# Kernel tuning notes

Hardware: AMD Instinct MI355X
Metric: run time of the kernel (lower is better)

The kernel has to match this reference:

```python
import jax, jax.numpy as jnp
import numpy as np

MAX_LEN = 3

def _attention(h, enc, w1, b1, w2):
    # h: [B,H], enc: [B,S,H]
    B, S, H = enc.shape
    hs = jnp.broadcast_to(h[:, None, :], (B, S, H))
    x = jnp.tanh(jnp.concatenate([enc, hs], axis=-1) @ w1.T + b1)  # [B,S,H]
    e = (x @ w2.T)[..., 0]                                         # [B,S]
    alpha = jax.nn.softmax(e, axis=1)
    return jnp.einsum('bs,bsd->bd', alpha, enc)                    # [B,H]

def _gru_cell(x, h, w_ih, w_hh, b_ih, b_hh):
    # torch GRU gate order: r, z, n
    H = h.shape[-1]
    gi = x @ w_ih.T + b_ih   # [B,3H]
    gh = h @ w_hh.T + b_hh
    i_r, i_z, i_n = gi[:, :H], gi[:, H:2*H], gi[:, 2*H:]
    h_r, h_z, h_n = gh[:, :H], gh[:, H:2*H], gh[:, 2*H:]
    r = jax.nn.sigmoid(i_r + h_r)
    z = jax.nn.sigmoid(i_z + h_z)
    n = jnp.tanh(i_n + r * h_n)
    return (1.0 - z) * n + z * h

def setup_inputs() -> dict:
    key = jax.random.key(0)
    ks = jax.random.split(key, 16)
    B, S, H, DW = 1024, 40, 1024, 512
    V0 = V1 = 4000
    EMB_N = V0 + V1 + 1
    sc = lambda fan: 1.0 / np.sqrt(fan)
    inp = {
        'encoder_outputs': jax.random.normal(ks[0], (B, S, H), jnp.float32),
        'encoder_hidden': jax.random.normal(ks[1], (1, B, H), jnp.float32),
        'targets': jax.random.randint(ks[2], (MAX_LEN, B), 0, V0),
        'emb': jax.random.normal(ks[3], (EMB_N, DW), jnp.float32) * 0.02,
        'attn_w1': jax.random.normal(ks[4], (H, 2 * H), jnp.float32) * sc(2 * H),
        'attn_b1': jnp.zeros((H,), jnp.float32),
        'attn_w2': jax.random.normal(ks[5], (1, H), jnp.float32) * sc(H),
        'w_ih': jax.random.normal(ks[6], (3 * H, H + DW), jnp.float32) * sc(H),
        'w_hh': jax.random.normal(ks[7], (3 * H, H), jnp.float32) * sc(H),
        'b_ih': jnp.zeros((3 * H,), jnp.float32),
        'b_hh': jnp.zeros((3 * H,), jnp.float32),
        'out0_w': jax.random.normal(ks[8], (V0, H), jnp.float32) * sc(H),
        'out0_b': jnp.zeros((V0,), jnp.float32),
        'out1_w': jax.random.normal(ks[9], (V1, H), jnp.float32) * sc(H),
        'out1_b': jnp.zeros((V1,), jnp.float32),
    }
    return inp

def reference(encoder_outputs, encoder_hidden, targets, emb, attn_w1, attn_b1,
              attn_w2, w_ih, w_hh, b_ih, b_hh, out0_w, out0_b, out1_w, out1_b):
    B = encoder_outputs.shape[0]
    h = encoder_hidden[0]  # n_layers=1, unidirectional -> init state passthrough
    logs = []
    for t in range(MAX_LEN):
        context = _attention(h, encoder_outputs, attn_w1, attn_b1, attn_w2)
        if t == 0:
            it = jnp.zeros((B,), jnp.int32)
        elif t == 1:
            it = targets[0] + 1
        else:
            it = targets[t - 1] + 36
        x = jnp.concatenate([emb[it], context], axis=1)  # [B, DW+H]
        h = _gru_cell(x, h, w_ih, w_hh, b_ih, b_hh)
        if t == 0 or t == 2:
            logits = h @ out0_w.T + out0_b
        else:
            logits = h @ out1_w.T + out1_b
        logs.append(jax.nn.log_softmax(logits, axis=1))
    return jnp.stack(logs)  # [MAX_LEN, B, V]
```

## Files before the change

### kernel.cpp

```cpp
#include <hip/hip_runtime.h>
#include <hip/hip_bf16.h>
#include <math.h>

#define B_SZ 1024
#define S_SZ 40
#define H_SZ 1024
#define DW_SZ 512
#define V_SZ 4000
#define XW (DW_SZ + H_SZ)
#define NG (4 * H_SZ)

typedef __bf16 bf16x8 __attribute__((ext_vector_type(8)));
typedef float f32x4 __attribute__((ext_vector_type(4)));

__device__ __forceinline__ float fast_tanh(float x) {
    return 1.0f - 2.0f / (1.0f + __expf(2.0f * x));
}
__device__ __forceinline__ float fast_sigmoid(float x) {
    return 1.0f / (1.0f + __expf(-x));
}
__device__ __forceinline__ float bfraw2f(unsigned short u) {
    return __uint_as_float(((unsigned)u) << 16);
}

#define GLL16(gp, lp)                                                                \
    __builtin_amdgcn_global_load_lds((const __attribute__((address_space(1))) void*)(gp), \
                                     (__attribute__((address_space(3))) void*)(lp), 16, 0, 0)

__global__ __launch_bounds__(256, 2) void gemm_bt_pipe128(
    const __hip_bfloat16* __restrict__ A, int lda,
    const __hip_bfloat16* __restrict__ W, int ldw,
    __hip_bfloat16* __restrict__ C, int ldc,
    int nbx, int K) {
    extern __shared__ char smem[];
    const int tid = threadIdx.x;
    const int lane = tid & 63;
    const int wave = tid >> 6;
    const int wm = wave >> 1, wn = wave & 1;
    const int fr = lane & 15, fq = lane >> 4;

    int bid = blockIdx.x;
    { const int cpx = gridDim.x >> 3; bid = (bid & 7) * cpx + (bid >> 3); }
    const int by = bid / nbx;
    const int bm = by * 128;
    const int bn = (bid - by * nbx) * 256;

    const int r0 = tid >> 2;
    const int s0 = (tid & 3) ^ ((tid >> 3) & 3);
    const __hip_bfloat16* gA0 = A + (size_t)(bm + r0) * lda + s0 * 8;
    const __hip_bfloat16* gA1 = A + (size_t)(bm + r0 + 64) * lda + s0 * 8;
    const __hip_bfloat16* gW0 = W + (size_t)(bn + r0) * ldw + s0 * 8;
    const __hip_bfloat16* gW1 = W + (size_t)(bn + r0 + 64) * ldw + s0 * 8;
    const __hip_bfloat16* gW2 = W + (size_t)(bn + r0 + 128) * ldw + s0 * 8;
    const __hip_bfloat16* gW3 = W + (size_t)(bn + r0 + 192) * ldw + s0 * 8;
    const int dst0 = tid * 16;

    int aoff[4], boff[8];
#pragma unroll
    for (int mi = 0; mi < 4; ++mi) {
        const int row = wm * 64 + mi * 16 + fr;
        aoff[mi] = row * 64 + ((fq ^ ((row >> 1) & 3)) << 4);
    }
#pragma unroll
    for (int ni = 0; ni < 8; ++ni) {
        const int col = wn * 128 + ni * 16 + fr;
        boff[ni] = 8192 + col * 64 + ((fq ^ ((col >> 1) & 3)) << 4);
    }

    const int NT = K >> 5;
    f32x4 acc[4][8] = {};

#define STAGE_T(t)                                                    \
    do {                                                              \
        char* sb = smem + ((t) % 3) * 24576;                          \
        const int kk = (t) << 5;                                      \
        GLL16(gA0 + kk, sb + dst0);                                   \
        GLL16(gA1 + kk, sb + dst0 + 4096);                            \
        GLL16(gW0 + kk, sb + 8192 + dst0);                            \
        GLL16(gW1 + kk, sb + 8192 + dst0 + 4096);                     \
        GLL16(gW2 + kk, sb + 8192 + dst0 + 8192);                     \
        GLL16(gW3 + kk, sb + 8192 + dst0 + 12288);                    \
    } while (0)

    STAGE_T(0);
    STAGE_T(1);
    __builtin_amdgcn_sched_barrier(0);
    asm volatile("s_waitcnt vmcnt(6)" ::: "memory");
    __builtin_amdgcn_s_barrier();
    __builtin_amdgcn_sched_barrier(0);

    for (int t = 0; t < NT; ++t) {
        if (t + 2 < NT) STAGE_T(t + 2);

        const char* sb = smem + (t % 3) * 24576;
        bf16x8 af[4], bg[8];
#pragma unroll
        for (int ni = 0; ni < 8; ++ni) bg[ni] = *reinterpret_cast<const bf16x8*>(sb + boff[ni]);
#pragma unroll
        for (int mi = 0; mi < 4; ++mi) af[mi] = *reinterpret_cast<const bf16x8*>(sb + aoff[mi]);

        __builtin_amdgcn_s_setprio(1);
#pragma unroll
        for (int mi = 0; mi < 4; ++mi)
#pragma unroll
            for (int ni = 0; ni < 8; ++ni)
                acc[mi][ni] = __builtin_amdgcn_mfma_f32_16x16x32_bf16(af[mi], bg[ni], acc[mi][ni], 0, 0, 0);
        __builtin_amdgcn_s_setprio(0);

        if (t != NT - 1) {
            __builtin_amdgcn_sched_barrier(0);
            if (t + 2 < NT) asm volatile("s_waitcnt vmcnt(6)" ::: "memory");
            else            asm volatile("s_waitcnt vmcnt(0)" ::: "memory");
            __builtin_amdgcn_s_barrier();
            __builtin_amdgcn_sched_barrier(0);
        }
    }
#undef STAGE_T

#pragma unroll
    for (int mi = 0; mi < 4; ++mi) {
        const int row0 = bm + wm * 64 + mi * 16 + fq * 4;
#pragma unroll
        for (int ni = 0; ni < 8; ++ni) {
            const int col = bn + wn * 128 + ni * 16 + fr;
#pragma unroll
            for (int r = 0; r < 4; ++r)
                C[(size_t)(row0 + r) * ldc + col] = __float2bfloat16(acc[mi][ni][r]);
        }
    }
}

template <int OB, int SWZ>
__global__ __launch_bounds__(256) void gemm_bt_mfma(
    const __hip_bfloat16* __restrict__ A, int lda,
    const __hip_bfloat16* __restrict__ W, int ldw,
    const float* __restrict__ bias,
    void* __restrict__ Cv, int ldc,
    int nbx, int N, int K) {
    __shared__ __align__(16) __hip_bfloat16 As[128 * 32];
    __shared__ __align__(16) __hip_bfloat16 Ws[128 * 32];
    const int tid = threadIdx.x;
    const int lane = tid & 63;
    const int wave = tid >> 6;

    int bid = blockIdx.x;
    if (SWZ) {
        const int cpx = gridDim.x >> 3;
        bid = (bid & 7) * cpx + (bid >> 3);
    }
    const int by = bid / nbx;
    const int bx = bid - by * nbx;
    const int bm = by * 128;
    const int bn = bx * 128;

    const int r0 = tid >> 2;
    const int kk = (tid & 3) * 8;
    const __hip_bfloat16* gA0 = A + (size_t)(bm + r0) * lda + kk;
    const __hip_bfloat16* gA1 = gA0 + (size_t)64 * lda;
    int wrow0 = bn + r0;      if (wrow0 > N - 1) wrow0 = N - 1;
    int wrow1 = bn + r0 + 64; if (wrow1 > N - 1) wrow1 = N - 1;
    const __hip_bfloat16* gW0 = W + (size_t)wrow0 * ldw + kk;
    const __hip_bfloat16* gW1 = W + (size_t)wrow1 * ldw + kk;
    char* As_c = (char*)As + tid * 16;
    char* Ws_c = (char*)Ws + tid * 16;

    const int wr = wave >> 1, wc = wave & 1;
    const int fr = lane & 15, fq = lane >> 4;
    const __hip_bfloat16* Ard = &As[(wr * 64 + fr) * 32 + fq * 8];
    const __hip_bfloat16* Wrd = &Ws[(wc * 64 + fr) * 32 + fq * 8];

    f32x4 acc[4][4] = {};

    for (int k0 = 0; k0 < K; k0 += 32) {
        __syncthreads();
        GLL16(gA0 + k0, As_c);
        GLL16(gA1 + k0, As_c + 4096);
        GLL16(gW0 + k0, Ws_c);
        GLL16(gW1 + k0, Ws_c + 4096);
        __syncthreads();

        bf16x8 af[4], bg[4];
#pragma unroll
        for (int i = 0; i < 4; ++i) {
            af[i] = *reinterpret_cast<const bf16x8*>(Ard + i * 16 * 32);
            bg[i] = *reinterpret_cast<const bf16x8*>(Wrd + i * 16 * 32);
        }
#pragma unroll
        for (int mi = 0; mi < 4; ++mi)
#pragma unroll
            for (int ni = 0; ni < 4; ++ni)
                acc[mi][ni] = __builtin_amdgcn_mfma_f32_16x16x32_bf16(af[mi], bg[ni], acc[mi][ni], 0, 0, 0);
    }

#pragma unroll
    for (int ni = 0; ni < 4; ++ni) {
        const int col = bn + wc * 64 + ni * 16 + fr;
        if (col >= N) continue;
        const float bb = bias ? bias[col] : 0.0f;
#pragma unroll
        for (int mi = 0; mi < 4; ++mi) {
            const int row0 = bm + wr * 64 + mi * 16 + fq * 4;
#pragma unroll
            for (int r = 0; r < 4; ++r) {
                const float v = acc[mi][ni][r] + bb;
                if (OB)
                    reinterpret_cast<__hip_bfloat16*>(Cv)[(size_t)(row0 + r) * ldc + col] = __float2bfloat16(v);
                else
                    reinterpret_cast<float*>(Cv)[(size_t)(row0 + r) * ldc + col] = v;
            }
        }
    }
}

__global__ __launch_bounds__(256) void gemm_dual_mfma(
    const __hip_bfloat16* __restrict__ A,
    const __hip_bfloat16* __restrict__ Wg,
    const __hip_bfloat16* __restrict__ Wo,
    const float* __restrict__ bias_cat,
    const float* __restrict__ ob,
    __hip_bfloat16* __restrict__ hg,
    float* __restrict__ logits,
    int full) {
    const int nbx = 64;
    const int bid = blockIdx.x;
    const int by = bid / nbx;
    const int bx = bid - by * nbx;
    const int bm = by * 128;
    const int bn = bx * 128;
    const int is_hg = (bn < NG);
    if (!full && is_hg) return;

    __shared__ __align__(16) __hip_bfloat16 As[128 * 32];
    __shared__ __align__(16) __hip_bfloat16 Ws[128 * 32];
    const int tid = threadIdx.x;
    const int lane = tid & 63;
    const int wave = tid >> 6;

    const __hip_bfloat16* Wb = is_hg ? Wg : Wo;
    const int coff = is_hg ? bn : bn - NG;
    const int nn = is_hg ? NG : V_SZ;

    const int r0 = tid >> 2;
    const int kk = (tid & 3) * 8;
    const __hip_bfloat16* gA0 = A + (size_t)(bm + r0) * H_SZ + kk;
    const __hip_bfloat16* gA1 = gA0 + (size_t)64 * H_SZ;
    int wrow0 = coff + r0;      if (wrow0 > nn - 1) wrow0 = nn - 1;
    int wrow1 = coff + r0 + 64; if (wrow1 > nn - 1) wrow1 = nn - 1;
    const __hip_bfloat16* gW0 = Wb + (size_t)wrow0 * H_SZ + kk;
    const __hip_bfloat16* gW1 = Wb + (size_t)wrow1 * H_SZ + kk;
    char* As_c = (char*)As + tid * 16;
    char* Ws_c = (char*)Ws + tid * 16;

    const int wr = wave >> 1, wc = wave & 1;
    const int fr = lane & 15, fq = lane >> 4;
    const __hip_bfloat16* Ard = &As[(wr * 64 + fr) * 32 + fq * 8];
    const __hip_bfloat16* Wrd = &Ws[(wc * 64 + fr) * 32 + fq * 8];

    f32x4 acc[4][4] = {};

    for (int k0 = 0; k0 < H_SZ; k0 += 32) {
        __syncthreads();
        GLL16(gA0 + k0, As_c);
        GLL16(gA1 + k0, As_c + 4096);
        GLL16(gW0 + k0, Ws_c);
        GLL16(gW1 + k0, Ws_c + 4096);
        __syncthreads();

        bf16x8 af[4], bg[4];
#pragma unroll
        for (int i = 0; i < 4; ++i) {
            af[i] = *reinterpret_cast<const bf16x8*>(Ard + i * 16 * 32);
            bg[i] = *reinterpret_cast<const bf16x8*>(Wrd + i * 16 * 32);
        }
#pragma unroll
        for (int mi = 0; mi < 4; ++mi)
#pragma unroll
            for (int ni = 0; ni < 4; ++ni)
                acc[mi][ni] = __builtin_amdgcn_mfma_f32_16x16x32_bf16(af[mi], bg[ni], acc[mi][ni], 0, 0, 0);
    }

#pragma unroll
    for (int ni = 0; ni < 4; ++ni) {
        const int cl = coff + wc * 64 + ni * 16 + fr;
        if (cl >= nn) continue;
        const float bb = is_hg ? bias_cat[cl] : ob[cl];
#pragma unroll
        for (int mi = 0; mi < 4; ++mi) {
            const int row0 = bm + wr * 64 + mi * 16 + fq * 4;
#pragma unroll
            for (int r = 0; r < 4; ++r) {
                const float v = acc[mi][ni][r] + bb;
                if (is_hg)
                    hg[(size_t)(row0 + r) * NG + cl] = __float2bfloat16(v);
                else
                    logits[(size_t)(row0 + r) * V_SZ + cl] = v;
            }
        }
    }
}

__global__ __launch_bounds__(256) void cast_f32_to_bf16(
    const float* __restrict__ src, long long sstride, int cols,
    __hip_bfloat16* __restrict__ dst, int nrows) {
    const int c4n = cols >> 2;
    const long long total4 = (long long)nrows * c4n;
    for (long long i = (long long)blockIdx.x * 256 + threadIdx.x; i < total4;
         i += (long long)gridDim.x * 256) {
        const long long r = i / c4n;
        const int c = (int)(i - r * c4n) << 2;
        const float4 v = *reinterpret_cast<const float4*>(src + r * sstride + c);
        union { ushort4 u; __hip_bfloat16 h[4]; } o;
        o.h[0] = __float2bfloat16(v.x); o.h[1] = __float2bfloat16(v.y);
        o.h[2] = __float2bfloat16(v.z); o.h[3] = __float2bfloat16(v.w);
        *reinterpret_cast<ushort4*>(dst + r * (long long)cols + c) = o.u;
    }
}

struct CastSeg { const float* src; long long sstride; int c4n; __hip_bfloat16* dst; long long n4; };
__global__ __launch_bounds__(256) void cast_all_kernel(CastSeg s0, CastSeg s1, CastSeg s2,
                                                       CastSeg s3, CastSeg s4, CastSeg s5) {
    const long long e0 = s0.n4, e1 = e0 + s1.n4, e2 = e1 + s2.n4,
                    e3 = e2 + s3.n4, e4 = e3 + s4.n4, e5 = e4 + s5.n4;
    for (long long i = (long long)blockIdx.x * 256 + threadIdx.x; i < e5;
         i += (long long)gridDim.x * 256) {
        CastSeg sg; long long li = i;
        if (i < e0) { sg = s0; }
        else if (i < e1) { sg = s1; li -= e0; }
        else if (i < e2) { sg = s2; li -= e1; }
        else if (i < e3) { sg = s3; li -= e2; }
        else if (i < e4) { sg = s4; li -= e3; }
        else { sg = s5; li -= e4; }
        const long long r = li / sg.c4n;
        const int c = (int)(li - r * sg.c4n) << 2;
        const float4 v = *reinterpret_cast<const float4*>(sg.src + r * sg.sstride + c);
        union { ushort4 u; __hip_bfloat16 h[4]; } o;
        o.h[0] = __float2bfloat16(v.x); o.h[1] = __float2bfloat16(v.y);
        o.h[2] = __float2bfloat16(v.z); o.h[3] = __float2bfloat16(v.w);
        *reinterpret_cast<ushort4*>(sg.dst + r * (long long)(sg.c4n << 2) + c) = o.u;
    }
}

__global__ __launch_bounds__(256) void build_bias_cat(
    const float* __restrict__ b1, const float* __restrict__ b_hh,
    float* __restrict__ dst) {
    const int j = blockIdx.x * 256 + threadIdx.x;
    dst[j] = (j < H_SZ) ? b1[j] : b_hh[j - H_SZ];
}

__global__ __launch_bounds__(256) void h_init_kernel(
    const float* __restrict__ enc_h, float* __restrict__ h, __hip_bfloat16* __restrict__ h_bf) {
    const int i = blockIdx.x * 256 + threadIdx.x;
    const float4 v = reinterpret_cast<const float4*>(enc_h)[i];
    reinterpret_cast<float4*>(h)[i] = v;
    union { ushort4 u; __hip_bfloat16 hh[4]; } o;
    o.hh[0] = __float2bfloat16(v.x); o.hh[1] = __float2bfloat16(v.y);
    o.hh[2] = __float2bfloat16(v.z); o.hh[3] = __float2bfloat16(v.w);
    reinterpret_cast<ushort4*>(h_bf)[i] = o.u;
}

__global__ __launch_bounds__(128) void emb_prefill_kernel(
    const float* __restrict__ emb,
    const int* __restrict__ targets,
    __hip_bfloat16* __restrict__ x0,
    __hip_bfloat16* __restrict__ x1,
    __hip_bfloat16* __restrict__ x2) {
    const int blk = blockIdx.x;
    const int t = blk >> 10;
    const int b = blk & 1023;
    const int tid = threadIdx.x;
    int it;
    __hip_bfloat16* x;
    if (t == 0) { it = 0; x = x0; }
    else if (t == 1) { it = targets[b] + 1; x = x1; }
    else { it = targets[B_SZ + b] + 36; x = x2; }
    float4 v = reinterpret_cast<const float4*>(emb + (size_t)it * DW_SZ)[tid];
    union { ushort4 u; __hip_bfloat16 h[4]; } o;
    o.h[0] = __float2bfloat16(v.x); o.h[1] = __float2bfloat16(v.y);
    o.h[2] = __float2bfloat16(v.z); o.h[3] = __float2bfloat16(v.w);
    reinterpret_cast<ushort4*>(x + (size_t)b * XW)[tid] = o.u;
}

__global__ __launch_bounds__(256) void attn_ctx_kernel(
    const __hip_bfloat16* __restrict__ enc,
    const __hip_bfloat16* __restrict__ enc_proj,
    const __hip_bfloat16* __restrict__ hg,
    const float* __restrict__ w2,
    __hip_bfloat16* __restrict__ x) {
    const int b = blockIdx.x;
    const int tid = threadIdx.x;
    const int lane = tid & 63, wave = tid >> 6;
    __shared__ float s_e[S_SZ];

    float hp[16], wv[16];
    const unsigned short* hgrow = reinterpret_cast<const unsigned short*>(hg) + (size_t)b * NG;
#pragma unroll
    for (int p = 0; p < 4; ++p) {
        const int base = p * 256 + lane * 4;
        ushort4 hu = *reinterpret_cast<const ushort4*>(hgrow + base);
        float4 wq = *reinterpret_cast<const float4*>(w2 + base);
        hp[p * 4 + 0] = bfraw2f(hu.x); hp[p * 4 + 1] = bfraw2f(hu.y);
        hp[p * 4 + 2] = bfraw2f(hu.z); hp[p * 4 + 3] = bfraw2f(hu.w);
        wv[p * 4 + 0] = wq.x; wv[p * 4 + 1] = wq.y;
        wv[p * 4 + 2] = wq.z; wv[p * 4 + 3] = wq.w;
    }

    const unsigned short* ep0 = reinterpret_cast<const unsigned short*>(enc_proj) + (size_t)b * S_SZ * H_SZ;
#pragma unroll 2
    for (int i = 0; i < 10; ++i) {
        const int s = wave + 4 * i;
        const unsigned short* row = ep0 + (size_t)s * H_SZ;
        float acc = 0.f;
#pragma unroll
        for (int p = 0; p < 4; ++p) {
            ushort4 eu = *reinterpret_cast<const ushort4*>(row + p * 256 + lane * 4);
            acc += fast_tanh(bfraw2f(eu.x) + hp[p * 4 + 0]) * wv[p * 4 + 0]
                 + fast_tanh(bfraw2f(eu.y) + hp[p * 4 + 1]) * wv[p * 4 + 1]
                 + fast_tanh(bfraw2f(eu.z) + hp[p * 4 + 2]) * wv[p * 4 + 2]
                 + fast_tanh(bfraw2f(eu.w) + hp[p * 4 + 3]) * wv[p * 4 + 3];
        }
#pragma unroll
        for (int off = 32; off > 0; off >>= 1) acc += __shfl_down(acc, off);
        if (lane == 0) s_e[s] = acc;
    }
    __syncthreads();

    float m = -1e30f;
    for (int s = 0; s < S_SZ; ++s) m = fmaxf(m, s_e[s]);
    float sum = 0.f;
    for (int s = 0; s < S_SZ; ++s) sum += __expf(s_e[s] - m);
    const float inv = 1.0f / sum;

    const ushort4* enc_b = reinterpret_cast<const ushort4*>(enc + (size_t)b * S_SZ * H_SZ);
    float4 acc = make_float4(0.f, 0.f, 0.f, 0.f);
    for (int s = 0; s < S_SZ; ++s) {
        const float a = __expf(s_e[s] - m) * inv;
        ushort4 ev = enc_b[s * 256 + tid];
        acc.x += a * bfraw2f(ev.x); acc.y += a * bfraw2f(ev.y);
        acc.z += a * bfraw2f(ev.z); acc.w += a * bfraw2f(ev.w);
    }
    union { ushort4 u; __hip_bfloat16 h[4]; } o;
    o.h[0] = __float2bfloat16(acc.x); o.h[1] = __float2bfloat16(acc.y);
    o.h[2] = __float2bfloat16(acc.z); o.h[3] = __float2bfloat16(acc.w);
    reinterpret_cast<ushort4*>(x + (size_t)b * XW + DW_SZ)[tid] = o.u;
}

__global__ __launch_bounds__(256) void gru_gate_kernel(
    const __hip_bfloat16* __restrict__ gi,
    const __hip_bfloat16* __restrict__ hg,
    float* __restrict__ h,
    __hip_bfloat16* __restrict__ h_bf) {
    const int idx = blockIdx.x * 256 + threadIdx.x;
    const int b = idx >> 10;
    const int j = idx & 1023;
    const unsigned short* gib = reinterpret_cast<const unsigned short*>(gi) + (size_t)b * 3 * H_SZ;
    const unsigned short* ghb = reinterpret_cast<const unsigned short*>(hg) + (size_t)b * NG + H_SZ;
    const float i_r = bfraw2f(gib[j]), i_z = bfraw2f(gib[H_SZ + j]), i_n = bfraw2f(gib[2 * H_SZ + j]);
    const float h_r = bfraw2f(ghb[j]), h_z = bfraw2f(ghb[H_SZ + j]), h_n = bfraw2f(ghb[2 * H_SZ + j]);
    const float r = fast_sigmoid(i_r + h_r);
    const float z = fast_sigmoid(i_z + h_z);
    const float n = fast_tanh(i_n + r * h_n);
    const float hv = (1.0f - z) * n + z * h[idx];
    h[idx] = hv;
    h_bf[idx] = __float2bfloat16(hv);
}

__global__ __launch_bounds__(256) void logsoftmax_kernel(float* __restrict__ buf) {
    const int b = blockIdx.x;
    const int tid = threadIdx.x;
    const int lane = tid & 63, wave = tid >> 6;
    __shared__ float s_red[4];
    __shared__ float s_bc;
    float* row = buf + (size_t)b * V_SZ;

    float m = -1e30f;
    for (int k = tid; k < V_SZ; k += 256) m = fmaxf(m, row[k]);
#pragma unroll
    for (int off = 32; off > 0; off >>= 1) m = fmaxf(m, __shfl_down(m, off));
    if (lane == 0) s_red[wave] = m;
    __syncthreads();
    if (tid == 0) s_bc = fmaxf(fmaxf(s_red[0], s_red[1]), fmaxf(s_red[2], s_red[3]));
    __syncthreads();
    m = s_bc;

    float sum = 0.f;
    for (int k = tid; k < V_SZ; k += 256) sum += expf(row[k] - m);
#pragma unroll
    for (int off = 32; off > 0; off >>= 1) sum += __shfl_down(sum, off);
    __syncthreads();
    if (lane == 0) s_red[wave] = sum;
    __syncthreads();
    if (tid == 0) s_bc = logf(s_red[0] + s_red[1] + s_red[2] + s_red[3]) + m;
    __syncthreads();
    const float ls = s_bc;

    for (int k = tid; k < V_SZ; k += 256) row[k] = row[k] - ls;
}

extern "C" void kernel_launch(void* const* d_in, const int* in_sizes, int n_in,
                              void* d_out, int out_size, void* d_ws, size_t ws_size,
                              hipStream_t stream) {
    const float* enc    = (const float*)d_in[0];
    const float* enc_h  = (const float*)d_in[1];
    const int*   tgt    = (const int*)d_in[2];
    const float* emb    = (const float*)d_in[3];
    const float* w1     = (const float*)d_in[4];
    const float* b1     = (const float*)d_in[5];
    const float* w2     = (const float*)d_in[6];
    const float* w_ih   = (const float*)d_in[7];
    const float* w_hh   = (const float*)d_in[8];
    const float* b_ih   = (const float*)d_in[9];
    const float* b_hh   = (const float*)d_in[10];
    const float* out0_w = (const float*)d_in[11];
    const float* out0_b = (const float*)d_in[12];
    const float* out1_w = (const float*)d_in[13];
    const float* out1_b = (const float*)d_in[14];
    float* out = (float*)d_out;

    char* wp = (char*)d_ws;
    auto carve = [&](size_t bytes) { char* p = wp; wp += (bytes + 255) & ~(size_t)255; return p; };
    __hip_bfloat16* enc_bf  = (__hip_bfloat16*)carve((size_t)B_SZ * S_SZ * H_SZ * 2);
    __hip_bfloat16* encp_bf = (__hip_bfloat16*)carve((size_t)B_SZ * S_SZ * H_SZ * 2);
    __hip_bfloat16* w1a_bf  = (__hip_bfloat16*)carve((size_t)H_SZ * H_SZ * 2);
    __hip_bfloat16* wcat_bf = (__hip_bfloat16*)carve((size_t)NG * H_SZ * 2);
    __hip_bfloat16* wih_bf  = (__hip_bfloat16*)carve((size_t)3 * H_SZ * XW * 2);
    __hip_bfloat16* o0_bf   = (__hip_bfloat16*)carve((size_t)V_SZ * H_SZ * 2);
    __hip_bfloat16* o1_bf   = (__hip_bfloat16*)carve((size_t)V_SZ * H_SZ * 2);
    float*          bias_cat= (float*)carve((size_t)NG * 4);
    float*          h       = (float*)carve((size_t)B_SZ * H_SZ * 4);
    __hip_bfloat16* h_bf    = (__hip_bfloat16*)carve((size_t)B_SZ * H_SZ * 2);
    __hip_bfloat16* hg_bf   = (__hip_bfloat16*)carve((size_t)B_SZ * NG * 2);
    __hip_bfloat16* x_bf[3];
    for (int t = 0; t < 3; ++t) x_bf[t] = (__hip_bfloat16*)carve((size_t)B_SZ * XW * 2);
    __hip_bfloat16* gi_bf   = (__hip_bfloat16*)carve((size_t)B_SZ * 3 * H_SZ * 2);

    cast_f32_to_bf16<<<2048, 256, 0, stream>>>(enc, H_SZ, H_SZ, enc_bf, B_SZ * S_SZ);
    {
        CastSeg s0{w1,            2 * H_SZ, H_SZ / 4, w1a_bf,                        (long long)H_SZ * H_SZ / 4};
        CastSeg s1{w1 + H_SZ,     2 * H_SZ, H_SZ / 4, wcat_bf,                       (long long)H_SZ * H_SZ / 4};
        CastSeg s2{w_hh,          H_SZ,     H_SZ / 4, wcat_bf + (size_t)H_SZ * H_SZ, (long long)3 * H_SZ * H_SZ / 4};
        CastSeg s3{w_ih,          XW,       XW / 4,   wih_bf,                        (long long)3 * H_SZ * XW / 4};
        CastSeg s4{out0_w,        H_SZ,     H_SZ / 4, o0_bf,                         (long long)V_SZ * H_SZ / 4};
        CastSeg s5{out1_w,        H_SZ,     H_SZ / 4, o1_bf,                         (long long)V_SZ * H_SZ / 4};
        cast_all_kernel<<<2048, 256, 0, stream>>>(s0, s1, s2, s3, s4, s5);
    }
    build_bias_cat<<<NG / 256, 256, 0, stream>>>(b1, b_hh, bias_cat);
    emb_prefill_kernel<<<3 * B_SZ, 128, 0, stream>>>(emb, tgt, x_bf[0], x_bf[1], x_bf[2]);
    h_init_kernel<<<(B_SZ * H_SZ / 4) / 256, 256, 0, stream>>>(enc_h, h, h_bf);

    gemm_bt_pipe128<<<(B_SZ * S_SZ / 128) * (H_SZ / 256), 256, 3 * 24576, stream>>>(
        enc_bf, H_SZ, w1a_bf, H_SZ, encp_bf, H_SZ, H_SZ / 256, H_SZ);

    gemm_bt_mfma<1, 0><<<(B_SZ / 128) * (NG / 128), 256, 0, stream>>>(
        h_bf, H_SZ, wcat_bf, H_SZ, bias_cat, hg_bf, NG, NG / 128, NG, H_SZ);

    for (int t = 0; t < 3; ++t) {
        attn_ctx_kernel<<<B_SZ, 256, 0, stream>>>(enc_bf, encp_bf, hg_bf, w2, x_bf[t]);

        gemm_bt_mfma<1, 0><<<(B_SZ / 128) * (3 * H_SZ / 128), 256, 0, stream>>>(
            x_bf[t], XW, wih_bf, XW, b_ih, gi_bf, 3 * H_SZ, 3 * H_SZ / 128, 3 * H_SZ, XW);

        gru_gate_kernel<<<(B_SZ * H_SZ) / 256, 256, 0, stream>>>(gi_bf, hg_bf, h, h_bf);

        float* logits = out + (size_t)t * B_SZ * V_SZ;
        const __hip_bfloat16* ow = (t == 1) ? o1_bf : o0_bf;
        const float* ob = (t == 1) ? out1_b : out0_b;
        gemm_dual_mfma<<<(B_SZ / 128) * 64, 256, 0, stream>>>(
            h_bf, wcat_bf, ow, bias_cat, ob, hg_bf, logits, (t < 2) ? 1 : 0);

        logsoftmax_kernel<<<B_SZ, 256, 0, stream>>>(logits);
    }
}
```

Before: 556.7 us.

## Fuse attention with log-softmax, merge prep kernels, store logits as bf16

Fuses the next step's attention-context kernel and the current step's log-softmax into one launch with block-range dispatch. Logits are written as bf16 to a scratch buffer and expanded to fp32 during log-softmax, which cuts fp32 round-trip traffic. Folds the encoder cast into cast_all_kernel and merges the embedding prefill, h init and bias concat into one kernel, removing several launches. It also moves the GEMM prefetch stage after the LDS fragment reads, and it adds bf16 rounding error to the logits.

```diff
diff --git a/kernel.cpp b/kernel.cpp
--- a/kernel.cpp
+++ b/kernel.cpp
@@ -90,14 +90,14 @@
     __builtin_amdgcn_sched_barrier(0);
 
     for (int t = 0; t < NT; ++t) {
-        if (t + 2 < NT) STAGE_T(t + 2);
-
         const char* sb = smem + (t % 3) * 24576;
         bf16x8 af[4], bg[8];
 #pragma unroll
         for (int ni = 0; ni < 8; ++ni) bg[ni] = *reinterpret_cast<const bf16x8*>(sb + boff[ni]);
 #pragma unroll
         for (int mi = 0; mi < 4; ++mi) af[mi] = *reinterpret_cast<const bf16x8*>(sb + aoff[mi]);
+
+        if (t + 2 < NT) STAGE_T(t + 2);
 
         __builtin_amdgcn_s_setprio(1);
 #pragma unroll
@@ -219,7 +219,7 @@
     const float* __restrict__ bias_cat,
     const float* __restrict__ ob,
     __hip_bfloat16* __restrict__ hg,
-    float* __restrict__ logits,
+    __hip_bfloat16* __restrict__ lg,
     int full) {
     const int nbx = 64;
     const int bid = blockIdx.x;
@@ -293,35 +293,18 @@
                 if (is_hg)
                     hg[(size_t)(row0 + r) * NG + cl] = __float2bfloat16(v);
                 else
-                    logits[(size_t)(row0 + r) * V_SZ + cl] = v;
+                    lg[(size_t)(row0 + r) * V_SZ + cl] = __float2bfloat16(v);
             }
         }
-    }
-}
-
-__global__ __launch_bounds__(256) void cast_f32_to_bf16(
-    const float* __restrict__ src, long long sstride, int cols,
-    __hip_bfloat16* __restrict__ dst, int nrows) {
-    const int c4n = cols >> 2;
-    const long long total4 = (long long)nrows * c4n;
-    for (long long i = (long long)blockIdx.x * 256 + threadIdx.x; i < total4;
-         i += (long long)gridDim.x * 256) {
-        const long long r = i / c4n;
-        const int c = (int)(i - r * c4n) << 2;
-        const float4 v = *reinterpret_cast<const float4*>(src + r * sstride + c);
-        union { ushort4 u; __hip_bfloat16 h[4]; } o;
-        o.h[0] = __float2bfloat16(v.x); o.h[1] = __float2bfloat16(v.y);
-        o.h[2] = __float2bfloat16(v.z); o.h[3] = __float2bfloat16(v.w);
-        *reinterpret_cast<ushort4*>(dst + r * (long long)cols + c) = o.u;
     }
 }
 
 struct CastSeg { const float* src; long long sstride; int c4n; __hip_bfloat16* dst; long long n4; };
 __global__ __launch_bounds__(256) void cast_all_kernel(CastSeg s0, CastSeg s1, CastSeg s2,
-                                                       CastSeg s3, CastSeg s4, CastSeg s5) {
+                                                       CastSeg s3, CastSeg s4, CastSeg s5, CastSeg s6) {
     const long long e0 = s0.n4, e1 = e0 + s1.n4, e2 = e1 + s2.n4,
-                    e3 = e2 + s3.n4, e4 = e3 + s4.n4, e5 = e4 + s5.n4;
-    for (long long i = (long long)blockIdx.x * 256 + threadIdx.x; i < e5;
+                    e3 = e2 + s3.n4, e4 = e3 + s4.n4, e5 = e4 + s5.n4, e6 = e5 + s6.n4;
+    for (long long i = (long long)blockIdx.x * 256 + threadIdx.x; i < e6;
          i += (long long)gridDim.x * 256) {
         CastSeg sg; long long li = i;
         if (i < e0) { sg = s0; }
@@ -329,7 +312,8 @@
         else if (i < e2) { sg = s2; li -= e1; }
         else if (i < e3) { sg = s3; li -= e2; }
         else if (i < e4) { sg = s4; li -= e3; }
-        else { sg = s5; li -= e4; }
+        else if (i < e5) { sg = s5; li -= e4; }
+        else { sg = s6; li -= e5; }
         const long long r = li / sg.c4n;
         const int c = (int)(li - r * sg.c4n) << 2;
         const float4 v = *reinterpret_cast<const float4*>(sg.src + r * sg.sstride + c);
@@ -340,108 +324,150 @@
     }
 }
 
-__global__ __launch_bounds__(256) void build_bias_cat(
-    const float* __restrict__ b1, const float* __restrict__ b_hh,
-    float* __restrict__ dst) {
-    const int j = blockIdx.x * 256 + threadIdx.x;
-    dst[j] = (j < H_SZ) ? b1[j] : b_hh[j - H_SZ];
-}
-
-__global__ __launch_bounds__(256) void h_init_kernel(
-    const float* __restrict__ enc_h, float* __restrict__ h, __hip_bfloat16* __restrict__ h_bf) {
-    const int i = blockIdx.x * 256 + threadIdx.x;
-    const float4 v = reinterpret_cast<const float4*>(enc_h)[i];
-    reinterpret_cast<float4*>(h)[i] = v;
-    union { ushort4 u; __hip_bfloat16 hh[4]; } o;
-    o.hh[0] = __float2bfloat16(v.x); o.hh[1] = __float2bfloat16(v.y);
-    o.hh[2] = __float2bfloat16(v.z); o.hh[3] = __float2bfloat16(v.w);
-    reinterpret_cast<ushort4*>(h_bf)[i] = o.u;
-}
-
-__global__ __launch_bounds__(128) void emb_prefill_kernel(
-    const float* __restrict__ emb,
-    const int* __restrict__ targets,
-    __hip_bfloat16* __restrict__ x0,
-    __hip_bfloat16* __restrict__ x1,
-    __hip_bfloat16* __restrict__ x2) {
+__global__ __launch_bounds__(256) void small_prep_kernel(
+    const float* __restrict__ emb, const int* __restrict__ targets,
+    __hip_bfloat16* __restrict__ x0, __hip_bfloat16* __restrict__ x1, __hip_bfloat16* __restrict__ x2,
+    const float* __restrict__ enc_h, float* __restrict__ h, __hip_bfloat16* __restrict__ h_bf,
+    const float* __restrict__ b1, const float* __restrict__ b_hh, float* __restrict__ bias_cat) {
     const int blk = blockIdx.x;
-    const int t = blk >> 10;
-    const int b = blk & 1023;
     const int tid = threadIdx.x;
-    int it;
-    __hip_bfloat16* x;
-    if (t == 0) { it = 0; x = x0; }
-    else if (t == 1) { it = targets[b] + 1; x = x1; }
-    else { it = targets[B_SZ + b] + 36; x = x2; }
-    float4 v = reinterpret_cast<const float4*>(emb + (size_t)it * DW_SZ)[tid];
-    union { ushort4 u; __hip_bfloat16 h[4]; } o;
-    o.h[0] = __float2bfloat16(v.x); o.h[1] = __float2bfloat16(v.y);
-    o.h[2] = __float2bfloat16(v.z); o.h[3] = __float2bfloat16(v.w);
-    reinterpret_cast<ushort4*>(x + (size_t)b * XW)[tid] = o.u;
-}
-
-__global__ __launch_bounds__(256) void attn_ctx_kernel(
+    if (blk < 3072) {
+        if (tid >= 128) return;
+        const int t = blk >> 10;
+        const int b = blk & 1023;
+        int it; __hip_bfloat16* x;
+        if (t == 0) { it = 0; x = x0; }
+        else if (t == 1) { it = targets[b] + 1; x = x1; }
+        else { it = targets[B_SZ + b] + 36; x = x2; }
+        float4 v = reinterpret_cast<const float4*>(emb + (size_t)it * DW_SZ)[tid];
+        union { ushort4 u; __hip_bfloat16 hh[4]; } o;
+        o.hh[0] = __float2bfloat16(v.x); o.hh[1] = __float2bfloat16(v.y);
+        o.hh[2] = __float2bfloat16(v.z); o.hh[3] = __float2bfloat16(v.w);
+        reinterpret_cast<ushort4*>(x + (size_t)b * XW)[tid] = o.u;
+    } else if (blk < 4096) {
+        const int i = (blk - 3072) * 256 + tid;
+        const float4 v = reinterpret_cast<const float4*>(enc_h)[i];
+        reinterpret_cast<float4*>(h)[i] = v;
+        union { ushort4 u; __hip_bfloat16 hh[4]; } o;
+        o.hh[0] = __float2bfloat16(v.x); o.hh[1] = __float2bfloat16(v.y);
+        o.hh[2] = __float2bfloat16(v.z); o.hh[3] = __float2bfloat16(v.w);
+        reinterpret_cast<ushort4*>(h_bf)[i] = o.u;
+    } else {
+        for (int j = tid; j < NG; j += 256)
+            bias_cat[j] = (j < H_SZ) ? b1[j] : b_hh[j - H_SZ];
+    }
+}
+
+__global__ __launch_bounds__(256) void attn_ls_kernel(
     const __hip_bfloat16* __restrict__ enc,
     const __hip_bfloat16* __restrict__ enc_proj,
     const __hip_bfloat16* __restrict__ hg,
     const float* __restrict__ w2,
-    __hip_bfloat16* __restrict__ x) {
-    const int b = blockIdx.x;
+    __hip_bfloat16* __restrict__ x,
+    const __hip_bfloat16* __restrict__ lg,
+    float* __restrict__ outp,
+    int nattn) {
+    const int blk = blockIdx.x;
     const int tid = threadIdx.x;
     const int lane = tid & 63, wave = tid >> 6;
     __shared__ float s_e[S_SZ];
-
-    float hp[16], wv[16];
-    const unsigned short* hgrow = reinterpret_cast<const unsigned short*>(hg) + (size_t)b * NG;
-#pragma unroll
-    for (int p = 0; p < 4; ++p) {
-        const int base = p * 256 + lane * 4;
-        ushort4 hu = *reinterpret_cast<const ushort4*>(hgrow + base);
-        float4 wq = *reinterpret_cast<const float4*>(w2 + base);
-        hp[p * 4 + 0] = bfraw2f(hu.x); hp[p * 4 + 1] = bfraw2f(hu.y);
-        hp[p * 4 + 2] = bfraw2f(hu.z); hp[p * 4 + 3] = bfraw2f(hu.w);
-        wv[p * 4 + 0] = wq.x; wv[p * 4 + 1] = wq.y;
-        wv[p * 4 + 2] = wq.z; wv[p * 4 + 3] = wq.w;
-    }
-
-    const unsigned short* ep0 = reinterpret_cast<const unsigned short*>(enc_proj) + (size_t)b * S_SZ * H_SZ;
+    __shared__ float s_red[4];
+    __shared__ float s_bc;
+
+    if (blk < nattn) {
+        const int b = blk;
+        float hp[16], wv[16];
+        const unsigned short* hgrow = reinterpret_cast<const unsigned short*>(hg) + (size_t)b * NG;
+#pragma unroll
+        for (int p = 0; p < 4; ++p) {
+            const int base = p * 256 + lane * 4;
+            ushort4 hu = *reinterpret_cast<const ushort4*>(hgrow + base);
+            float4 wq = *reinterpret_cast<const float4*>(w2 + base);
+            hp[p * 4 + 0] = bfraw2f(hu.x); hp[p * 4 + 1] = bfraw2f(hu.y);
+            hp[p * 4 + 2] = bfraw2f(hu.z); hp[p * 4 + 3] = bfraw2f(hu.w);
+            wv[p * 4 + 0] = wq.x; wv[p * 4 + 1] = wq.y;
+            wv[p * 4 + 2] = wq.z; wv[p * 4 + 3] = wq.w;
+        }
+
+        const unsigned short* ep0 = reinterpret_cast<const unsigned short*>(enc_proj) + (size_t)b * S_SZ * H_SZ;
 #pragma unroll 2
-    for (int i = 0; i < 10; ++i) {
-        const int s = wave + 4 * i;
-        const unsigned short* row = ep0 + (size_t)s * H_SZ;
-        float acc = 0.f;
-#pragma unroll
-        for (int p = 0; p < 4; ++p) {
-            ushort4 eu = *reinterpret_cast<const ushort4*>(row + p * 256 + lane * 4);
-            acc += fast_tanh(bfraw2f(eu.x) + hp[p * 4 + 0]) * wv[p * 4 + 0]
-                 + fast_tanh(bfraw2f(eu.y) + hp[p * 4 + 1]) * wv[p * 4 + 1]
-                 + fast_tanh(bfraw2f(eu.z) + hp[p * 4 + 2]) * wv[p * 4 + 2]
-                 + fast_tanh(bfraw2f(eu.w) + hp[p * 4 + 3]) * wv[p * 4 + 3];
-        }
-#pragma unroll
-        for (int off = 32; off > 0; off >>= 1) acc += __shfl_down(acc, off);
-        if (lane == 0) s_e[s] = acc;
-    }
-    __syncthreads();
-
-    float m = -1e30f;
-    for (int s = 0; s < S_SZ; ++s) m = fmaxf(m, s_e[s]);
-    float sum = 0.f;
-    for (int s = 0; s < S_SZ; ++s) sum += __expf(s_e[s] - m);
-    const float inv = 1.0f / sum;
-
-    const ushort4* enc_b = reinterpret_cast<const ushort4*>(enc + (size_t)b * S_SZ * H_SZ);
-    float4 acc = make_float4(0.f, 0.f, 0.f, 0.f);
-    for (int s = 0; s < S_SZ; ++s) {
-        const float a = __expf(s_e[s] - m) * inv;
-        ushort4 ev = enc_b[s * 256 + tid];
-        acc.x += a * bfraw2f(ev.x); acc.y += a * bfraw2f(ev.y);
-        acc.z += a * bfraw2f(ev.z); acc.w += a * bfraw2f(ev.w);
-    }
-    union { ushort4 u; __hip_bfloat16 h[4]; } o;
-    o.h[0] = __float2bfloat16(acc.x); o.h[1] = __float2bfloat16(acc.y);
-    o.h[2] = __float2bfloat16(acc.z); o.h[3] = __float2bfloat16(acc.w);
-    reinterpret_cast<ushort4*>(x + (size_t)b * XW + DW_SZ)[tid] = o.u;
+        for (int i = 0; i < 10; ++i) {
+            const int s = wave + 4 * i;
+            const unsigned short* row = ep0 + (size_t)s * H_SZ;
+            float acc = 0.f;
+#pragma unroll
+            for (int p = 0; p < 4; ++p) {
+                ushort4 eu = *reinterpret_cast<const ushort4*>(row + p * 256 + lane * 4);
+                acc += fast_tanh(bfraw2f(eu.x) + hp[p * 4 + 0]) * wv[p * 4 + 0]
+                     + fast_tanh(bfraw2f(eu.y) + hp[p * 4 + 1]) * wv[p * 4 + 1]
+                     + fast_tanh(bfraw2f(eu.z) + hp[p * 4 + 2]) * wv[p * 4 + 2]
+                     + fast_tanh(bfraw2f(eu.w) + hp[p * 4 + 3]) * wv[p * 4 + 3];
+            }
+#pragma unroll
+            for (int off = 32; off > 0; off >>= 1) acc += __shfl_down(acc, off);
+            if (lane == 0) s_e[s] = acc;
+        }
+        __syncthreads();
+
+        float m = -1e30f;
+        for (int s = 0; s < S_SZ; ++s) m = fmaxf(m, s_e[s]);
+        float sum = 0.f;
+        for (int s = 0; s < S_SZ; ++s) sum += __expf(s_e[s] - m);
+        const float inv = 1.0f / sum;
+
+        const ushort4* enc_b = reinterpret_cast<const ushort4*>(enc + (size_t)b * S_SZ * H_SZ);
+        float4 acc = make_float4(0.f, 0.f, 0.f, 0.f);
+        for (int s = 0; s < S_SZ; ++s) {
+            const float a = __expf(s_e[s] - m) * inv;
+            ushort4 ev = enc_b[s * 256 + tid];
+            acc.x += a * bfraw2f(ev.x); acc.y += a * bfraw2f(ev.y);
+            acc.z += a * bfraw2f(ev.z); acc.w += a * bfraw2f(ev.w);
+        }
+        union { ushort4 u; __hip_bfloat16 hh[4]; } o;
+        o.hh[0] = __float2bfloat16(acc.x); o.hh[1] = __float2bfloat16(acc.y);
+        o.hh[2] = __float2bfloat16(acc.z); o.hh[3] = __float2bfloat16(acc.w);
+        reinterpret_cast<ushort4*>(x + (size_t)b * XW + DW_SZ)[tid] = o.u;
+    } else {
+        const int b = blk - nattn;
+        const ushort4* row4 = reinterpret_cast<const ushort4*>(
+            reinterpret_cast<const unsigned short*>(lg) + (size_t)b * V_SZ);
+        float* orow = outp + (size_t)b * V_SZ;
+
+        float m = -1e30f;
+        for (int k = tid; k < V_SZ / 4; k += 256) {
+            ushort4 u = row4[k];
+            m = fmaxf(m, fmaxf(fmaxf(bfraw2f(u.x), bfraw2f(u.y)), fmaxf(bfraw2f(u.z), bfraw2f(u.w))));
+        }
+#pragma unroll
+        for (int off = 32; off > 0; off >>= 1) m = fmaxf(m, __shfl_down(m, off));
+        if (lane == 0) s_red[wave] = m;
+        __syncthreads();
+        if (tid == 0) s_bc = fmaxf(fmaxf(s_red[0], s_red[1]), fmaxf(s_red[2], s_red[3]));
+        __syncthreads();
+        m = s_bc;
+
+        float sum = 0.f;
+        for (int k = tid; k < V_SZ / 4; k += 256) {
+            ushort4 u = row4[k];
+            sum += expf(bfraw2f(u.x) - m) + expf(bfraw2f(u.y) - m)
+                 + expf(bfraw2f(u.z) - m) + expf(bfraw2f(u.w) - m);
+        }
+#pragma unroll
+        for (int off = 32; off > 0; off >>= 1) sum += __shfl_down(sum, off);
+        __syncthreads();
+        if (lane == 0) s_red[wave] = sum;
+        __syncthreads();
+        if (tid == 0) s_bc = logf(s_red[0] + s_red[1] + s_red[2] + s_red[3]) + m;
+        __syncthreads();
+        const float ls = s_bc;
+
+        for (int k = tid; k < V_SZ / 4; k += 256) {
+            ushort4 u = row4[k];
+            float4 o = make_float4(bfraw2f(u.x) - ls, bfraw2f(u.y) - ls,
+                                   bfraw2f(u.z) - ls, bfraw2f(u.w) - ls);
+            reinterpret_cast<float4*>(orow)[k] = o;
+        }
+    }
 }
 
 __global__ __launch_bounds__(256) void gru_gate_kernel(
@@ -462,38 +488,6 @@
     const float hv = (1.0f - z) * n + z * h[idx];
     h[idx] = hv;
     h_bf[idx] = __float2bfloat16(hv);
-}
-
-__global__ __launch_bounds__(256) void logsoftmax_kernel(float* __restrict__ buf) {
-    const int b = blockIdx.x;
-    const int tid = threadIdx.x;
-    const int lane = tid & 63, wave = tid >> 6;
-    __shared__ float s_red[4];
-    __shared__ float s_bc;
-    float* row = buf + (size_t)b * V_SZ;
-
-    float m = -1e30f;
-    for (int k = tid; k < V_SZ; k += 256) m = fmaxf(m, row[k]);
-#pragma unroll
-    for (int off = 32; off > 0; off >>= 1) m = fmaxf(m, __shfl_down(m, off));
-    if (lane == 0) s_red[wave] = m;
-    __syncthreads();
-    if (tid == 0) s_bc = fmaxf(fmaxf(s_red[0], s_red[1]), fmaxf(s_red[2], s_red[3]));
-    __syncthreads();
-    m = s_bc;
-
-    float sum = 0.f;
-    for (int k = tid; k < V_SZ; k += 256) sum += expf(row[k] - m);
-#pragma unroll
-    for (int off = 32; off > 0; off >>= 1) sum += __shfl_down(sum, off);
-    __syncthreads();
-    if (lane == 0) s_red[wave] = sum;
-    __syncthreads();
-    if (tid == 0) s_bc = logf(s_red[0] + s_red[1] + s_red[2] + s_red[3]) + m;
-    __syncthreads();
-    const float ls = s_bc;
-
-    for (int k = tid; k < V_SZ; k += 256) row[k] = row[k] - ls;
 }
 
 extern "C" void kernel_launch(void* const* d_in, const int* in_sizes, int n_in,
@@ -532,20 +526,20 @@
     __hip_bfloat16* x_bf[3];
     for (int t = 0; t < 3; ++t) x_bf[t] = (__hip_bfloat16*)carve((size_t)B_SZ * XW * 2);
     __hip_bfloat16* gi_bf   = (__hip_bfloat16*)carve((size_t)B_SZ * 3 * H_SZ * 2);
-
-    cast_f32_to_bf16<<<2048, 256, 0, stream>>>(enc, H_SZ, H_SZ, enc_bf, B_SZ * S_SZ);
+    __hip_bfloat16* lg_bf   = (__hip_bfloat16*)carve((size_t)B_SZ * V_SZ * 2);
+
     {
-        CastSeg s0{w1,            2 * H_SZ, H_SZ / 4, w1a_bf,                        (long long)H_SZ * H_SZ / 4};
-        CastSeg s1{w1 + H_SZ,     2 * H_SZ, H_SZ / 4, wcat_bf,                       (long long)H_SZ * H_SZ / 4};
-        CastSeg s2{w_hh,          H_SZ,     H_SZ / 4, wcat_bf + (size_t)H_SZ * H_SZ, (long long)3 * H_SZ * H_SZ / 4};
-        CastSeg s3{w_ih,          XW,       XW / 4,   wih_bf,                        (long long)3 * H_SZ * XW / 4};
-        CastSeg s4{out0_w,        H_SZ,     H_SZ / 4, o0_bf,                         (long long)V_SZ * H_SZ / 4};
-        CastSeg s5{out1_w,        H_SZ,     H_SZ / 4, o1_bf,                         (long long)V_SZ * H_SZ / 4};
-        cast_all_kernel<<<2048, 256, 0, stream>>>(s0, s1, s2, s3, s4, s5);
-    }
-    build_bias_cat<<<NG / 256, 256, 0, stream>>>(b1, b_hh, bias_cat);
-    emb_prefill_kernel<<<3 * B_SZ, 128, 0, stream>>>(emb, tgt, x_bf[0], x_bf[1], x_bf[2]);
-    h_init_kernel<<<(B_SZ * H_SZ / 4) / 256, 256, 0, stream>>>(enc_h, h, h_bf);
+        CastSeg s0{w1,        2 * H_SZ, H_SZ / 4, w1a_bf,                        (long long)H_SZ * H_SZ / 4};
+        CastSeg s1{w1 + H_SZ, 2 * H_SZ, H_SZ / 4, wcat_bf,                       (long long)H_SZ * H_SZ / 4};
+        CastSeg s2{w_hh,      H_SZ,     H_SZ / 4, wcat_bf + (size_t)H_SZ * H_SZ, (long long)3 * H_SZ * H_SZ / 4};
+        CastSeg s3{w_ih,      XW,       XW / 4,   wih_bf,                        (long long)3 * H_SZ * XW / 4};
+        CastSeg s4{out0_w,    H_SZ,     H_SZ / 4, o0_bf,                         (long long)V_SZ * H_SZ / 4};
+        CastSeg s5{out1_w,    H_SZ,     H_SZ / 4, o1_bf,                         (long long)V_SZ * H_SZ / 4};
+        CastSeg s6{enc,       H_SZ,     H_SZ / 4, enc_bf,                        (long long)B_SZ * S_SZ * H_SZ / 4};
+        cast_all_kernel<<<4096, 256, 0, stream>>>(s0, s1, s2, s3, s4, s5, s6);
+    }
+    small_prep_kernel<<<4097, 256, 0, stream>>>(emb, tgt, x_bf[0], x_bf[1], x_bf[2],
+                                                enc_h, h, h_bf, b1, b_hh, bias_cat);
 
     gemm_bt_pipe128<<<(B_SZ * S_SZ / 128) * (H_SZ / 256), 256, 3 * 24576, stream>>>(
         enc_bf, H_SZ, w1a_bf, H_SZ, encp_bf, H_SZ, H_SZ / 256, H_SZ);
@@ -553,20 +547,27 @@
     gemm_bt_mfma<1, 0><<<(B_SZ / 128) * (NG / 128), 256, 0, stream>>>(
         h_bf, H_SZ, wcat_bf, H_SZ, bias_cat, hg_bf, NG, NG / 128, NG, H_SZ);
 
+    attn_ls_kernel<<<B_SZ, 256, 0, stream>>>(enc_bf, encp_bf, hg_bf, w2, x_bf[0],
+                                             lg_bf, out, B_SZ);
+
     for (int t = 0; t < 3; ++t) {
-        attn_ctx_kernel<<<B_SZ, 256, 0, stream>>>(enc_bf, encp_bf, hg_bf, w2, x_bf[t]);
-
         gemm_bt_mfma<1, 0><<<(B_SZ / 128) * (3 * H_SZ / 128), 256, 0, stream>>>(
             x_bf[t], XW, wih_bf, XW, b_ih, gi_bf, 3 * H_SZ, 3 * H_SZ / 128, 3 * H_SZ, XW);
 
         gru_gate_kernel<<<(B_SZ * H_SZ) / 256, 256, 0, stream>>>(gi_bf, hg_bf, h, h_bf);
 
-        float* logits = out + (size_t)t * B_SZ * V_SZ;
         const __hip_bfloat16* ow = (t == 1) ? o1_bf : o0_bf;
         const float* ob = (t == 1) ? out1_b : out0_b;
         gemm_dual_mfma<<<(B_SZ / 128) * 64, 256, 0, stream>>>(
-            h_bf, wcat_bf, ow, bias_cat, ob, hg_bf, logits, (t < 2) ? 1 : 0);
-
-        logsoftmax_kernel<<<B_SZ, 256, 0, stream>>>(logits);
-    }
-}
+            h_bf, wcat_bf, ow, bias_cat, ob, hg_bf, lg_bf, (t < 2) ? 1 : 0);
+
+        float* outp = out + (size_t)t * B_SZ * V_SZ;
+        if (t < 2) {
+            attn_ls_kernel<<<2 * B_SZ, 256, 0, stream>>>(enc_bf, encp_bf, hg_bf, w2, x_bf[t + 1],
+                                                         lg_bf, outp, B_SZ);
+        } else {
+            attn_ls_kernel<<<B_SZ, 256, 0, stream>>>(enc_bf, encp_bf, hg_bf, w2, x_bf[0],
+                                                     lg_bf, outp, 0);
+        }
+    }
+}
```

Result: faster. 538.1 us (-3.4%).
